# Kernel tuning notes

Measured on AMD Instinct MI355X. Metric: run time of the kernel, lower is better.

The kernel has to match this reference:

```python
import jax, jax.numpy as jnp
import numpy as np

B, M, N = 4, 1024, 32768

def setup_inputs() -> dict:
    key = jax.random.key(0)
    k1, k2 = jax.random.split(key)
    keypoints = jax.random.normal(k1, (B, 3, M), dtype=jnp.float32)
    pc = jax.random.normal(k2, (B, 3, N), dtype=jnp.float32)
    return {"keypoints": keypoints, "pc": pc}

def reference(keypoints, pc):
    # Pairwise Euclidean distances via the expanded quadratic form:
    # ||k - p||^2 = ||k||^2 + ||p||^2 - 2 k.p  -> avoids the [B,3,M,N] tensor.
    k2 = jnp.sum(keypoints * keypoints, axis=1)            # [B, M]
    p2 = jnp.sum(pc * pc, axis=1)                          # [B, N]
    cross = jnp.einsum("bdm,bdn->bmn", keypoints, pc)     # [B, M, N]
    d2 = k2[:, :, None] + p2[:, None, :] - 2.0 * cross     # [B, M, N]
    dist = jnp.sqrt(jnp.maximum(d2, 0.0))
    min_dist = jnp.min(dist, axis=2)                       # [B, M]
    return jnp.mean(min_dist)
```

## Files before the change

### kernel.cpp

```cpp
#include <hip/hip_runtime.h>
#include <math.h>

#define BATCH 4
#define M 1024
#define N 32768
#define NSPLIT 128
#define CHUNK (N / NSPLIT)
#define KPT 4
#define TPB 256

__global__ void p2p_init(unsigned* __restrict__ wsmin) {
    int i = blockIdx.x * blockDim.x + threadIdx.x;
    if (i < BATCH * M) wsmin[i] = 0x7F800000u;
}

__global__ __launch_bounds__(TPB) void p2p_partial(
        const float* __restrict__ kp, const float* __restrict__ pc,
        unsigned* __restrict__ wsmin) {
    __shared__ __align__(16) float px[CHUNK];
    __shared__ __align__(16) float py[CHUNK];
    __shared__ __align__(16) float pz[CHUNK];

    const int b = blockIdx.x / NSPLIT;
    const int c = blockIdx.x % NSPLIT;
    const int t = threadIdx.x;

    const float* pcb = pc + (size_t)b * 3 * N + c * CHUNK;
    px[t] = pcb[t];
    py[t] = pcb[N + t];
    pz[t] = pcb[2 * N + t];

    const float* kpb = kp + (size_t)b * 3 * M;
    float kx[KPT], ky[KPT], kz[KPT], md[KPT];
#pragma unroll
    for (int k = 0; k < KPT; ++k) {
        int m = t + k * TPB;
        kx[k] = kpb[m];
        ky[k] = kpb[M + m];
        kz[k] = kpb[2 * M + m];
        md[k] = INFINITY;
    }
    __syncthreads();

#pragma unroll 1
    for (int j = 0; j < CHUNK; j += 4) {
        float4 vx = *(const float4*)&px[j];
        float4 vy = *(const float4*)&py[j];
        float4 vz = *(const float4*)&pz[j];
        float X[4] = {vx.x, vx.y, vx.z, vx.w};
        float Y[4] = {vy.x, vy.y, vy.z, vy.w};
        float Z[4] = {vz.x, vz.y, vz.z, vz.w};
#pragma unroll
        for (int p = 0; p < 4; ++p) {
#pragma unroll
            for (int k = 0; k < KPT; ++k) {
                float dx = kx[k] - X[p];
                float dy = ky[k] - Y[p];
                float dz = kz[k] - Z[p];
                float d2 = fmaf(dx, dx, fmaf(dy, dy, dz * dz));
                md[k] = fminf(md[k], d2);
            }
        }
    }

#pragma unroll
    for (int k = 0; k < KPT; ++k) {
        atomicMin(&wsmin[b * M + t + k * TPB], __float_as_uint(md[k]));
    }
}

__global__ __launch_bounds__(1024) void p2p_reduce(
        const unsigned* __restrict__ wsmin, float* __restrict__ out) {
    __shared__ float sbuf[1024 / 64];
    const int t = threadIdx.x;
    float s = 0.f;
#pragma unroll
    for (int i = t; i < BATCH * M; i += 1024)
        s += sqrtf(__uint_as_float(wsmin[i]));
#pragma unroll
    for (int off = 32; off > 0; off >>= 1) s += __shfl_down(s, off, 64);
    if ((t & 63) == 0) sbuf[t >> 6] = s;
    __syncthreads();
    if (t == 0) {
        float tot = 0.f;
#pragma unroll
        for (int w = 0; w < 1024 / 64; ++w) tot += sbuf[w];
        out[0] = tot / (float)(BATCH * M);
    }
}

extern "C" void kernel_launch(void* const* d_in, const int* in_sizes, int n_in,
                              void* d_out, int out_size, void* d_ws, size_t ws_size,
                              hipStream_t stream) {
    const float* kp = (const float*)d_in[0];
    const float* pc = (const float*)d_in[1];
    float* out = (float*)d_out;
    unsigned* wsmin = (unsigned*)d_ws;

    p2p_init<<<(BATCH * M + 255) / 256, 256, 0, stream>>>(wsmin);
    p2p_partial<<<BATCH * NSPLIT, TPB, 0, stream>>>(kp, pc, wsmin);
    p2p_reduce<<<1, 1024, 0, stream>>>(wsmin, out);
}
```

Baseline: 77.20 us.

## Use expanded dot-product distance form and fuse final reduction via last-block ticket

The inner loop now computes k·p - 0.5|p|^2 with three FMAs per pair and tracks a running max, using a precomputed per-point norm term in shared memory. This replaces the per-pair subtractions and squares. The separate reduce kernel is removed: each block takes an atomic ticket after a threadfence, and the last block sums the square roots of the minima. The expanded form can lose precision through cancellation, and the ticket scheme relies on correct memory ordering.

```diff
diff --git a/kernel.cpp b/kernel.cpp
--- a/kernel.cpp
+++ b/kernel.cpp
@@ -9,36 +9,43 @@
 #define KPT 4
 #define TPB 256
 
-__global__ void p2p_init(unsigned* __restrict__ wsmin) {
+__global__ void p2p_init(unsigned* __restrict__ ws) {
     int i = blockIdx.x * blockDim.x + threadIdx.x;
-    if (i < BATCH * M) wsmin[i] = 0x7F800000u;
+    if (i < BATCH * M) ws[i] = 0x7F800000u;
+    else if (i == BATCH * M) ws[i] = 0u;
 }
 
-__global__ __launch_bounds__(TPB) void p2p_partial(
+__global__ __launch_bounds__(TPB) void p2p_main(
         const float* __restrict__ kp, const float* __restrict__ pc,
-        unsigned* __restrict__ wsmin) {
+        unsigned* __restrict__ ws, float* __restrict__ out) {
     __shared__ __align__(16) float px[CHUNK];
     __shared__ __align__(16) float py[CHUNK];
     __shared__ __align__(16) float pz[CHUNK];
+    __shared__ __align__(16) float pw[CHUNK];
+    __shared__ float sbuf[TPB / 64];
+    __shared__ int lastflag;
 
     const int b = blockIdx.x / NSPLIT;
     const int c = blockIdx.x % NSPLIT;
     const int t = threadIdx.x;
 
     const float* pcb = pc + (size_t)b * 3 * N + c * CHUNK;
-    px[t] = pcb[t];
-    py[t] = pcb[N + t];
-    pz[t] = pcb[2 * N + t];
+    {
+        float x = pcb[t], y = pcb[N + t], z = pcb[2 * N + t];
+        px[t] = x; py[t] = y; pz[t] = z;
+        pw[t] = -0.5f * fmaf(x, x, fmaf(y, y, z * z));
+    }
 
     const float* kpb = kp + (size_t)b * 3 * M;
-    float kx[KPT], ky[KPT], kz[KPT], md[KPT];
+    float kx[KPT], ky[KPT], kz[KPT], k2[KPT], mq[KPT];
 #pragma unroll
     for (int k = 0; k < KPT; ++k) {
         int m = t + k * TPB;
         kx[k] = kpb[m];
         ky[k] = kpb[M + m];
         kz[k] = kpb[2 * M + m];
-        md[k] = INFINITY;
+        k2[k] = fmaf(kx[k], kx[k], fmaf(ky[k], ky[k], kz[k] * kz[k]));
+        mq[k] = -INFINITY;
     }
     __syncthreads();
 
@@ -47,45 +54,52 @@
         float4 vx = *(const float4*)&px[j];
         float4 vy = *(const float4*)&py[j];
         float4 vz = *(const float4*)&pz[j];
+        float4 vw = *(const float4*)&pw[j];
         float X[4] = {vx.x, vx.y, vx.z, vx.w};
         float Y[4] = {vy.x, vy.y, vy.z, vy.w};
         float Z[4] = {vz.x, vz.y, vz.z, vz.w};
+        float W[4] = {vw.x, vw.y, vw.z, vw.w};
 #pragma unroll
-        for (int p = 0; p < 4; ++p) {
-#pragma unroll
-            for (int k = 0; k < KPT; ++k) {
-                float dx = kx[k] - X[p];
-                float dy = ky[k] - Y[p];
-                float dz = kz[k] - Z[p];
-                float d2 = fmaf(dx, dx, fmaf(dy, dy, dz * dz));
-                md[k] = fminf(md[k], d2);
-            }
+        for (int k = 0; k < KPT; ++k) {
+            float q0 = fmaf(kz[k], Z[0], fmaf(ky[k], Y[0], fmaf(kx[k], X[0], W[0])));
+            float q1 = fmaf(kz[k], Z[1], fmaf(ky[k], Y[1], fmaf(kx[k], X[1], W[1])));
+            float q2 = fmaf(kz[k], Z[2], fmaf(ky[k], Y[2], fmaf(kx[k], X[2], W[2])));
+            float q3 = fmaf(kz[k], Z[3], fmaf(ky[k], Y[3], fmaf(kx[k], X[3], W[3])));
+            mq[k] = fmaxf(fmaxf(mq[k], q0), q1);
+            mq[k] = fmaxf(fmaxf(mq[k], q2), q3);
         }
     }
 
 #pragma unroll
     for (int k = 0; k < KPT; ++k) {
-        atomicMin(&wsmin[b * M + t + k * TPB], __float_as_uint(md[k]));
+        float d2 = fmaxf(fmaf(-2.0f, mq[k], k2[k]), 0.0f);
+        atomicMin(&ws[b * M + t + k * TPB], __float_as_uint(d2));
     }
-}
 
-__global__ __launch_bounds__(1024) void p2p_reduce(
-        const unsigned* __restrict__ wsmin, float* __restrict__ out) {
-    __shared__ float sbuf[1024 / 64];
-    const int t = threadIdx.x;
-    float s = 0.f;
+    __threadfence();
+    if (t == 0) {
+        unsigned ticket = atomicAdd(&ws[BATCH * M], 1u);
+        lastflag = (ticket == (unsigned)(gridDim.x - 1)) ? 1 : 0;
+    }
+    __syncthreads();
+    if (lastflag) {
+        float s = 0.f;
 #pragma unroll
-    for (int i = t; i < BATCH * M; i += 1024)
-        s += sqrtf(__uint_as_float(wsmin[i]));
+        for (int i = t; i < BATCH * M; i += TPB) {
+            unsigned u = __hip_atomic_load(&ws[i], __ATOMIC_RELAXED,
+                                           __HIP_MEMORY_SCOPE_AGENT);
+            s += sqrtf(__uint_as_float(u));
+        }
 #pragma unroll
-    for (int off = 32; off > 0; off >>= 1) s += __shfl_down(s, off, 64);
-    if ((t & 63) == 0) sbuf[t >> 6] = s;
-    __syncthreads();
-    if (t == 0) {
-        float tot = 0.f;
+        for (int off = 32; off > 0; off >>= 1) s += __shfl_down(s, off, 64);
+        if ((t & 63) == 0) sbuf[t >> 6] = s;
+        __syncthreads();
+        if (t == 0) {
+            float tot = 0.f;
 #pragma unroll
-        for (int w = 0; w < 1024 / 64; ++w) tot += sbuf[w];
-        out[0] = tot / (float)(BATCH * M);
+            for (int w = 0; w < TPB / 64; ++w) tot += sbuf[w];
+            out[0] = tot / (float)(BATCH * M);
+        }
     }
 }
 
@@ -95,9 +109,8 @@
     const float* kp = (const float*)d_in[0];
     const float* pc = (const float*)d_in[1];
     float* out = (float*)d_out;
-    unsigned* wsmin = (unsigned*)d_ws;
+    unsigned* ws = (unsigned*)d_ws;
 
-    p2p_init<<<(BATCH * M + 255) / 256, 256, 0, stream>>>(wsmin);
-    p2p_partial<<<BATCH * NSPLIT, TPB, 0, stream>>>(kp, pc, wsmin);
-    p2p_reduce<<<1, 1024, 0, stream>>>(wsmin, out);
+    p2p_init<<<(BATCH * M + 1 + TPB - 1) / TPB, TPB, 0, stream>>>(ws);
+    p2p_main<<<BATCH * NSPLIT, TPB, 0, stream>>>(kp, pc, ws, out);
 }
```

Result: slower. 102.3 us (+32.6%).

## Use expanded dot-product form with keypoint-group blocks and drop atomics

Applied to the files above, without the earlier changes.

Rewrites the main kernel to compute k·p - |p|^2/2 and take a max, which needs 3 FMAs per pair instead of 3 subtracts plus 3 FMAs. Each block now holds 16 keypoints in registers and streams a quarter of the point cloud straight from global memory. Per-block results are reduced in shared memory and written to a partial buffer per split, so the init kernel and the atomics go away. The tail kernel takes the min across the 4 splits. The expanded quadratic form risks cancellation error, and every block rereads the point cloud from global memory or cache.

```diff
diff --git a/kernel.cpp b/kernel.cpp
--- a/kernel.cpp
+++ b/kernel.cpp
@@ -4,79 +4,101 @@
 #define BATCH 4
 #define M 1024
 #define N 32768
-#define NSPLIT 128
-#define CHUNK (N / NSPLIT)
-#define KPT 4
+#define MG 16
+#define NMG (M / MG)
+#define CSPLIT 4
+#define NPC (N / CSPLIT)
 #define TPB 256
+#define ROWS (BATCH * M)
 
-__global__ void p2p_init(unsigned* __restrict__ wsmin) {
-    int i = blockIdx.x * blockDim.x + threadIdx.x;
-    if (i < BATCH * M) wsmin[i] = 0x7F800000u;
-}
 
-__global__ __launch_bounds__(TPB) void p2p_partial(
+__global__ __launch_bounds__(TPB) void p2p_main(
         const float* __restrict__ kp, const float* __restrict__ pc,
-        unsigned* __restrict__ wsmin) {
-    __shared__ __align__(16) float px[CHUNK];
-    __shared__ __align__(16) float py[CHUNK];
-    __shared__ __align__(16) float pz[CHUNK];
+        float* __restrict__ pmin) {
+    const int c  = blockIdx.x & (CSPLIT - 1);
+    const int mg = (blockIdx.x >> 2) & (NMG - 1);
+    const int b  = blockIdx.x >> 8;
+    const int t  = threadIdx.x;
 
-    const int b = blockIdx.x / NSPLIT;
-    const int c = blockIdx.x % NSPLIT;
-    const int t = threadIdx.x;
+    const float* kpb = kp + (size_t)b * 3 * M + mg * MG;
+    float skx[MG], sky[MG], skz[MG];
+#pragma unroll
+    for (int k = 0; k < MG; ++k) {
+        skx[k] = kpb[k];
+        sky[k] = kpb[M + k];
+        skz[k] = kpb[2 * M + k];
+    }
 
-    const float* pcb = pc + (size_t)b * 3 * N + c * CHUNK;
-    px[t] = pcb[t];
-    py[t] = pcb[N + t];
-    pz[t] = pcb[2 * N + t];
+    float mq[MG];
+#pragma unroll
+    for (int k = 0; k < MG; ++k) mq[k] = -INFINITY;
 
-    const float* kpb = kp + (size_t)b * 3 * M;
-    float kx[KPT], ky[KPT], kz[KPT], md[KPT];
+    const float* pcb = pc + (size_t)b * 3 * N + c * NPC;
+#pragma unroll 2
+    for (int g = 0; g < NPC / (TPB * 4); ++g) {
+        const int n = g * (TPB * 4) + t * 4;
+        float4 X4 = *(const float4*)&pcb[n];
+        float4 Y4 = *(const float4*)&pcb[N + n];
+        float4 Z4 = *(const float4*)&pcb[2 * N + n];
+        float xs[4] = {X4.x, X4.y, X4.z, X4.w};
+        float ys[4] = {Y4.x, Y4.y, Y4.z, Y4.w};
+        float zs[4] = {Z4.x, Z4.y, Z4.z, Z4.w};
+        float w[4];
 #pragma unroll
-    for (int k = 0; k < KPT; ++k) {
-        int m = t + k * TPB;
-        kx[k] = kpb[m];
-        ky[k] = kpb[M + m];
-        kz[k] = kpb[2 * M + m];
-        md[k] = INFINITY;
-    }
-    __syncthreads();
-
-#pragma unroll 1
-    for (int j = 0; j < CHUNK; j += 4) {
-        float4 vx = *(const float4*)&px[j];
-        float4 vy = *(const float4*)&py[j];
-        float4 vz = *(const float4*)&pz[j];
-        float X[4] = {vx.x, vx.y, vx.z, vx.w};
-        float Y[4] = {vy.x, vy.y, vy.z, vy.w};
-        float Z[4] = {vz.x, vz.y, vz.z, vz.w};
+        for (int p = 0; p < 4; ++p)
+            w[p] = -0.5f * fmaf(xs[p], xs[p],
+                                fmaf(ys[p], ys[p], zs[p] * zs[p]));
 #pragma unroll
-        for (int p = 0; p < 4; ++p) {
-#pragma unroll
-            for (int k = 0; k < KPT; ++k) {
-                float dx = kx[k] - X[p];
-                float dy = ky[k] - Y[p];
-                float dz = kz[k] - Z[p];
-                float d2 = fmaf(dx, dx, fmaf(dy, dy, dz * dz));
-                md[k] = fminf(md[k], d2);
-            }
+        for (int k = 0; k < MG; ++k) {
+            float q0 = fmaf(skz[k], zs[0], fmaf(sky[k], ys[0],
+                        fmaf(skx[k], xs[0], w[0])));
+            float q1 = fmaf(skz[k], zs[1], fmaf(sky[k], ys[1],
+                        fmaf(skx[k], xs[1], w[1])));
+            float q2 = fmaf(skz[k], zs[2], fmaf(sky[k], ys[2],
+                        fmaf(skx[k], xs[2], w[2])));
+            float q3 = fmaf(skz[k], zs[3], fmaf(sky[k], ys[3],
+                        fmaf(skx[k], xs[3], w[3])));
+            mq[k] = fmaxf(fmaxf(mq[k], q0), q1);
+            mq[k] = fmaxf(fmaxf(mq[k], q2), q3);
         }
     }
 
+    __shared__ float smax[MG][TPB + 1];
+    __shared__ float s2[MG][17];
 #pragma unroll
-    for (int k = 0; k < KPT; ++k) {
-        atomicMin(&wsmin[b * M + t + k * TPB], __float_as_uint(md[k]));
+    for (int k = 0; k < MG; ++k) smax[k][t] = mq[k];
+    __syncthreads();
+    {
+        const int r = t >> 4, s = t & 15;
+        float m = smax[r][s * 16];
+#pragma unroll
+        for (int j = 1; j < 16; ++j) m = fmaxf(m, smax[r][s * 16 + j]);
+        s2[r][s] = m;
+    }
+    __syncthreads();
+    if (t < MG) {
+        float m = s2[t][0];
+#pragma unroll
+        for (int j = 1; j < 16; ++j) m = fmaxf(m, s2[t][j]);
+        float kx = kpb[t], ky = kpb[M + t], kz = kpb[2 * M + t];
+        float k2 = fmaf(kx, kx, fmaf(ky, ky, kz * kz));
+        float d2 = fmaxf(fmaf(-2.0f, m, k2), 0.0f);
+        pmin[(size_t)c * ROWS + b * M + mg * MG + t] = d2;
     }
 }
 
-__global__ __launch_bounds__(1024) void p2p_reduce(
-        const unsigned* __restrict__ wsmin, float* __restrict__ out) {
-    __shared__ float sbuf[1024 / 64];
+__global__ __launch_bounds__(1024) void p2p_tail(
+        const float* __restrict__ pmin, float* __restrict__ out) {
+    __shared__ float sbuf[16];
     const int t = threadIdx.x;
     float s = 0.f;
 #pragma unroll
-    for (int i = t; i < BATCH * M; i += 1024)
-        s += sqrtf(__uint_as_float(wsmin[i]));
+    for (int i = 0; i < ROWS / 1024; ++i) {
+        int r = i * 1024 + t;
+        float v = fminf(fminf(pmin[r], pmin[ROWS + r]),
+                        fminf(pmin[2 * ROWS + r], pmin[3 * ROWS + r]));
+        s += sqrtf(v);
+    }
 #pragma unroll
     for (int off = 32; off > 0; off >>= 1) s += __shfl_down(s, off, 64);
     if ((t & 63) == 0) sbuf[t >> 6] = s;
@@ -84,8 +106,8 @@
     if (t == 0) {
         float tot = 0.f;
 #pragma unroll
-        for (int w = 0; w < 1024 / 64; ++w) tot += sbuf[w];
-        out[0] = tot / (float)(BATCH * M);
+        for (int w = 0; w < 16; ++w) tot += sbuf[w];
+        out[0] = tot / (float)ROWS;
     }
 }
 
@@ -95,9 +117,8 @@
     const float* kp = (const float*)d_in[0];
     const float* pc = (const float*)d_in[1];
     float* out = (float*)d_out;
-    unsigned* wsmin = (unsigned*)d_ws;
+    float* pmin = (float*)d_ws;
 
-    p2p_init<<<(BATCH * M + 255) / 256, 256, 0, stream>>>(wsmin);
-    p2p_partial<<<BATCH * NSPLIT, TPB, 0, stream>>>(kp, pc, wsmin);
-    p2p_reduce<<<1, 1024, 0, stream>>>(wsmin, out);
+    p2p_main<<<BATCH * NMG * CSPLIT, TPB, 0, stream>>>(kp, pc, pmin);
+    p2p_tail<<<1, 1024, 0, stream>>>(pmin, out);
 }
```

New measurement: 73.26 us. 5.1% less time.
